# Performance work log

Measured on AMD Instinct MI355X. Metric: run time of the kernel, lower is better.

Reference implementation:

```python
import jax, jax.numpy as jnp
import numpy as np

N, D, H, E = 8192, 1024, 4096, 8
LN_EPS = 1e-5


def setup_inputs() -> dict:
    key = jax.random.key(0)
    ks = jax.random.split(key, 7)
    s_in = 1.0 / np.sqrt(D)
    s_hid = 1.0 / np.sqrt(H)
    return {
        "x": jax.random.normal(ks[0], (N, D), dtype=jnp.float32),
        "gate_w": jax.random.uniform(ks[1], (E, D), jnp.float32, -s_in, s_in),
        "gate_b": jax.random.uniform(ks[2], (E,), jnp.float32, -s_in, s_in),
        "w1": jax.random.uniform(ks[3], (E, H, D), jnp.float32, -s_in, s_in),
        "b1": jax.random.uniform(ks[4], (E, H), jnp.float32, -s_in, s_in),
        "w2": jax.random.uniform(ks[5], (E, D, H), jnp.float32, -s_hid, s_hid),
        "b2": jax.random.uniform(ks[6], (E, D), jnp.float32, -s_hid, s_hid),
        "ln_w": jnp.ones((D,), jnp.float32),
        "ln_b": jnp.zeros((D,), jnp.float32),
        "top_k": 2,
    }


def reference(x, gate_w, gate_b, w1, b1, w2, b2, ln_w, ln_b, top_k):
    # Gating: softmax over experts, then top-k, then renormalizing softmax over the k scores
    gate_scores = jax.nn.softmax(x @ gate_w.T + gate_b, axis=-1)          # [N, E]
    topk_scores, topk_idx = jax.lax.top_k(gate_scores, top_k)             # [N, K]
    topk_scores = jax.nn.softmax(topk_scores, axis=-1)                    # [N, K]

    # Dense all-expert FFN (matches original: every expert runs on every token)
    h = jax.nn.relu(jnp.einsum('nd,ehd->neh', x, w1) + b1)                # [N, E, H]
    y = jnp.einsum('neh,edh->ned', h, w2) + b2                            # [N, E, D]

    # Per-token gather of the top-k expert outputs and weighted combine
    sel = jnp.take_along_axis(y, topk_idx[:, :, None], axis=1)            # [N, K, D]
    moe_out = jnp.sum(topk_scores[:, :, None] * sel, axis=1)              # [N, D]

    # Residual + LayerNorm
    r = x + moe_out
    mu = jnp.mean(r, axis=-1, keepdims=True)
    var = jnp.mean(jnp.square(r - mu), axis=-1, keepdims=True)
    return (r - mu) * jax.lax.rsqrt(var + LN_EPS) * ln_w + ln_b
```

## Files before the change

kernel.cpp:

```cpp
#include <hip/hip_runtime.h>
#include <hip/hip_bf16.h>
#include <stdint.h>

#define N_TOK 8192
#define DIM 1024
#define HID 4096
#define NEXP 8
#define NSLOT 16384
#define NBLK 64

typedef __attribute__((ext_vector_type(8))) __bf16 bf16x8;
typedef __attribute__((ext_vector_type(4))) float f32x4;

__device__ __forceinline__ unsigned short f2bf(float f) {
  unsigned int u = __float_as_uint(f);
  u += 0x7fff + ((u >> 16) & 1);
  return (unsigned short)(u >> 16);
}
__device__ __forceinline__ float bf2f(unsigned short s) {
  return __uint_as_float(((unsigned int)s) << 16);
}
__device__ __forceinline__ void async16(const void* g, void* l) {
  __builtin_amdgcn_global_load_lds((__attribute__((address_space(1))) void*)(g),
                                   (__attribute__((address_space(3))) void*)(l), 16, 0, 0);
}
#define MFMA16(a, b, c) __builtin_amdgcn_mfma_f32_16x16x32_bf16(a, b, c, 0, 0, 0)

__global__ void cvt_kernel(const float* __restrict__ src, unsigned short* __restrict__ dst,
                           int n4) {
  int i = blockIdx.x * 256 + threadIdx.x;
  int stride = gridDim.x * 256;
  for (; i < n4; i += stride) {
    float4 v = ((const float4*)src)[i];
    ushort4 o;
    o.x = f2bf(v.x); o.y = f2bf(v.y); o.z = f2bf(v.z); o.w = f2bf(v.w);
    ((ushort4*)dst)[i] = o;
  }
}

__global__ void gate_kernel(const float* __restrict__ x, const float* __restrict__ gw,
                            const float* __restrict__ gb, int* __restrict__ expert2,
                            float* __restrict__ score2) {
  int token = blockIdx.x * 4 + (threadIdx.x >> 6);
  int lane = threadIdx.x & 63;
  const float4* xr = (const float4*)(x + (size_t)token * DIM);
  float acc[NEXP];
#pragma unroll
  for (int e = 0; e < NEXP; ++e) acc[e] = 0.f;
#pragma unroll
  for (int it = 0; it < DIM / 4 / 64; ++it) {
    int d = it * 64 + lane;
    float4 xv = xr[d];
#pragma unroll
    for (int e = 0; e < NEXP; ++e) {
      float4 wv = ((const float4*)(gw + e * DIM))[d];
      acc[e] += xv.x * wv.x + xv.y * wv.y + xv.z * wv.z + xv.w * wv.w;
    }
  }
#pragma unroll
  for (int off = 32; off > 0; off >>= 1) {
#pragma unroll
    for (int e = 0; e < NEXP; ++e) acc[e] += __shfl_xor(acc[e], off, 64);
  }
  if (lane == 0) {
    float lg[NEXP], mx = -1e30f;
#pragma unroll
    for (int e = 0; e < NEXP; ++e) { lg[e] = acc[e] + gb[e]; mx = fmaxf(mx, lg[e]); }
    float p[NEXP], s = 0.f;
#pragma unroll
    for (int e = 0; e < NEXP; ++e) { p[e] = expf(lg[e] - mx); s += p[e]; }
    float inv = 1.f / s;
#pragma unroll
    for (int e = 0; e < NEXP; ++e) p[e] *= inv;
    int i0 = 0;
#pragma unroll
    for (int e = 1; e < NEXP; ++e) if (p[e] > p[i0]) i0 = e;
    int i1 = (i0 == 0) ? 1 : 0;
#pragma unroll
    for (int e = 0; e < NEXP; ++e) if (e != i0 && p[e] > p[i1]) i1 = e;
    float eb = expf(p[i1] - p[i0]);
    float dn = 1.f / (1.f + eb);
    expert2[token * 2] = i0;
    expert2[token * 2 + 1] = i1;
    score2[token * 2] = dn;
    score2[token * 2 + 1] = eb * dn;
  }
}

__global__ void hist_kernel(const int* __restrict__ expert2, int* __restrict__ hist) {
  __shared__ int lh[NEXP];
  int b = blockIdx.x, t = threadIdx.x;
  if (t < NEXP) lh[t] = 0;
  __syncthreads();
  atomicAdd(&lh[expert2[b * 256 + t]], 1);
  __syncthreads();
  if (t < NEXP) hist[b * NEXP + t] = lh[t];
}

__global__ void scan_kernel(const int* __restrict__ hist, int* __restrict__ cnt,
                            int* __restrict__ off_, int* __restrict__ base) {
  __shared__ int lh[NBLK * NEXP];
  __shared__ int ltot[NEXP];
  __shared__ int loff[NEXP];
  int t = threadIdx.x;
#pragma unroll
  for (int e = 0; e < NEXP; ++e) lh[t * NEXP + e] = hist[t * NEXP + e];
  __syncthreads();
  if (t < NEXP) {
    int s = 0;
    for (int b = 0; b < NBLK; ++b) { int v = lh[b * NEXP + t]; lh[b * NEXP + t] = s; s += v; }
    ltot[t] = s;
  }
  __syncthreads();
  if (t == 0) {
    int s = 0;
#pragma unroll
    for (int e = 0; e < NEXP; ++e) { loff[e] = s; s += ltot[e]; }
  }
  __syncthreads();
  if (t < NEXP) { cnt[t] = ltot[t]; off_[t] = loff[t]; }
#pragma unroll
  for (int e = 0; e < NEXP; ++e) base[t * NEXP + e] = loff[e] + lh[t * NEXP + e];
}

__global__ void assign_kernel(const int* __restrict__ expert2, const int* __restrict__ base,
                              int* __restrict__ slot_of, int* __restrict__ token_of) {
  __shared__ int lh[NEXP];
  int b = blockIdx.x, t = threadIdx.x;
  if (t < NEXP) lh[t] = 0;
  __syncthreads();
  int i = b * 256 + t;
  int e = expert2[i];
  int r = atomicAdd(&lh[e], 1);
  int slot = base[b * NEXP + e] + r;
  slot_of[i] = slot;
  token_of[slot] = i >> 1;
}

__global__ void gather_kernel(const float* __restrict__ x, const int* __restrict__ token_of,
                              unsigned short* __restrict__ xg) {
  int slot = blockIdx.x;
  int t = threadIdx.x;
  int n = token_of[slot];
  float4 v = *(const float4*)(x + (size_t)n * DIM + t * 4);
  ushort4 o;
  o.x = f2bf(v.x); o.y = f2bf(v.y); o.z = f2bf(v.z); o.w = f2bf(v.w);
  *(ushort4*)(xg + (size_t)slot * DIM + t * 4) = o;
}

template <int KLEN, int NLEN, bool RELU>
__global__ __launch_bounds__(512, 2) void gemm_r3(
    const unsigned short* __restrict__ A, const unsigned short* __restrict__ B,
    const float* __restrict__ bias, unsigned short* __restrict__ C,
    const int* __restrict__ cnt, const int* __restrict__ off_) {
  const int NB_N = NLEN / 128;
  const int NT = KLEN / 64;
  int panel = blockIdx.z * 8 + blockIdx.x;
  int e = panel / NB_N;
  int n0 = (panel % NB_N) * 128;
  int me = cnt[e];
  int m0 = blockIdx.y * 256;
  if (m0 >= me) return;
  int rb = off_[e] + m0;

  __shared__ unsigned short lds_[73728];

  int tid = threadIdx.x;
  int wave = tid >> 6, lane = tid & 63;
  int wm = wave >> 1, wn = wave & 1;
  int quad = lane >> 4, l16 = lane & 15;
  int x7 = l16 & 7;

  int crow = tid >> 3, kc = tid & 7;
  int sslot = kc ^ (crow & 7);
  const char* Ab = (const char*)A;
  const char* Bb = (const char*)(B + (size_t)e * NLEN * KLEN);
  uint32_t aof[4], bof[2];
#pragma unroll
  for (int j = 0; j < 4; ++j) {
    int gr = rb + j * 64 + crow;
    gr = gr > NSLOT - 1 ? NSLOT - 1 : gr;
    aof[j] = (uint32_t)gr * (KLEN * 2) + sslot * 16;
  }
#pragma unroll
  for (int j = 0; j < 2; ++j)
    bof[j] = (uint32_t)(n0 + j * 64 + crow) * (KLEN * 2) + sslot * 16;

#define STG_A2(sbuf, kb, j0)                                                  \
  {                                                                           \
    async16(Ab + aof[j0] + (kb), &lds_[(sbuf) * 16384 + ((j0)*512 + tid) * 8]); \
    async16(Ab + aof[(j0) + 1] + (kb),                                        \
            &lds_[(sbuf) * 16384 + (((j0) + 1) * 512 + tid) * 8]);            \
  }
#define STG_B1(sbuf, kb, j)                                                   \
  async16(Bb + bof[j] + (kb), &lds_[49152 + (sbuf) * 8192 + ((j)*512 + tid) * 8]);

  f32x4 acc[4][4];
#pragma unroll
  for (int i = 0; i < 4; ++i)
#pragma unroll
    for (int j = 0; j < 4; ++j) acc[i][j] = {0.f, 0.f, 0.f, 0.f};

  STG_A2(0, 0, 0); STG_A2(0, 0, 2); STG_B1(0, 0, 0); STG_B1(0, 0, 1);
  STG_A2(1, 128, 0); STG_A2(1, 128, 2); STG_B1(1, 128, 0); STG_B1(1, 128, 1);
  asm volatile("s_waitcnt vmcnt(6)" ::: "memory");
  __builtin_amdgcn_sched_barrier(0);
  __builtin_amdgcn_s_barrier();

  const int abase = (wm * 64 + l16) * 64;
  const int bbase = (wn * 64 + l16) * 64;
  const int q0s = (quad ^ x7) * 8;
  const int q1s = ((4 + quad) ^ x7) * 8;

  int cur = 0;
#pragma unroll 1
  for (int t = 0; t < NT; ++t) {
    const int stg = (cur >= 1) ? cur - 1 : 2;
    const unsigned short* pa = &lds_[cur * 16384];
    const unsigned short* pb = &lds_[49152 + cur * 8192];
    const uint32_t kb2 = (uint32_t)(t + 2) << 7;
    const bool pre = (t + 2 < NT);
    bf16x8 a0[4], b0[4], a1[4], b1[4];
#pragma unroll
    for (int mt = 0; mt < 4; ++mt) a0[mt] = *(const bf16x8*)&pa[abase + mt * 1024 + q0s];
#pragma unroll
    for (int nt = 0; nt < 4; ++nt) b0[nt] = *(const bf16x8*)&pb[bbase + nt * 1024 + q0s];
    if (pre) { STG_A2(stg, kb2, 0); STG_B1(stg, kb2, 0); }
#pragma unroll
    for (int mt = 0; mt < 4; ++mt) a1[mt] = *(const bf16x8*)&pa[abase + mt * 1024 + q1s];
#pragma unroll
    for (int nt = 0; nt < 4; ++nt) b1[nt] = *(const bf16x8*)&pb[bbase + nt * 1024 + q1s];
    if (pre) { STG_A2(stg, kb2, 2); STG_B1(stg, kb2, 1); }
    asm volatile("s_waitcnt lgkmcnt(8)" ::: "memory");
    __builtin_amdgcn_sched_barrier(0);
    __builtin_amdgcn_s_setprio(1);
#pragma unroll
    for (int mt = 0; mt < 4; ++mt)
#pragma unroll
      for (int nt = 0; nt < 4; ++nt) acc[mt][nt] = MFMA16(a0[mt], b0[nt], acc[mt][nt]);
    __builtin_amdgcn_s_setprio(0);
    asm volatile("s_waitcnt lgkmcnt(0)" ::: "memory");
    __builtin_amdgcn_sched_barrier(0);
    __builtin_amdgcn_s_setprio(1);
#pragma unroll
    for (int mt = 0; mt < 4; ++mt)
#pragma unroll
      for (int nt = 0; nt < 4; ++nt) acc[mt][nt] = MFMA16(a1[mt], b1[nt], acc[mt][nt]);
    __builtin_amdgcn_s_setprio(0);
    if (t + 1 < NT) {
      if (pre) {
        asm volatile("s_waitcnt vmcnt(6)" ::: "memory");
      } else {
        asm volatile("s_waitcnt vmcnt(0)" ::: "memory");
      }
    }
    __builtin_amdgcn_sched_barrier(0);
    __builtin_amdgcn_s_barrier();
    cur = (cur == 2) ? 0 : cur + 1;
  }
#undef STG_A2
#undef STG_B1

#pragma unroll
  for (int mt = 0; mt < 4; ++mt) {
#pragma unroll
    for (int r = 0; r < 4; ++r) {
      int mrow = wm * 64 + mt * 16 + quad * 4 + r;
      if (m0 + mrow < me) {
#pragma unroll
        for (int nt = 0; nt < 4; ++nt) {
          int col = n0 + wn * 64 + nt * 16 + l16;
          float v = acc[mt][nt][r] + bias[e * NLEN + col];
          if (RELU) v = fmaxf(v, 0.f);
          C[(size_t)(rb + mrow) * NLEN + col] = f2bf(v);
        }
      }
    }
  }
}

template <int KLEN, int NLEN, bool RELU>
__global__ __launch_bounds__(256, 4) void gemm_bt(
    const unsigned short* __restrict__ A, const void* __restrict__ Bptr,
    const float* __restrict__ bias, unsigned short* __restrict__ C,
    const int* __restrict__ cnt, const int* __restrict__ off_) {
  const int NB_N = NLEN / 128;
  int panel = blockIdx.z * 8 + blockIdx.x;
  int e = panel / NB_N;
  int n0 = (panel % NB_N) * 128;
  int me = cnt[e];
  int m0 = blockIdx.y * 128;
  if (m0 >= me) return;
  int rb = off_[e] + m0;

  __shared__ unsigned short lA[8192];
  __shared__ unsigned short lB[8192];

  int tid = threadIdx.x;
  int wave = tid >> 6, lane = tid & 63;
  int wm = (wave >> 1) * 64, wn = (wave & 1) * 64;
  int quad = lane >> 4, l16 = lane & 15;
  int x7 = l16 & 7;

  int arow[4], brow[4], akx[4], ldst[4];
#pragma unroll
  for (int i = 0; i < 4; ++i) {
    int c = i * 256 + tid;
    int row = c >> 3;
    akx[i] = (c & 7) ^ (row & 7);
    ldst[i] = c * 8;
    brow[i] = row;
    int grow = rb + row;
    arow[i] = (grow > NSLOT - 1) ? (NSLOT - 1) : grow;
  }

  f32x4 acc[4][4];
#pragma unroll
  for (int i = 0; i < 4; ++i)
#pragma unroll
    for (int j = 0; j < 4; ++j) acc[i][j] = {0.f, 0.f, 0.f, 0.f};

  const float* Bf = (const float*)Bptr + (size_t)e * NLEN * KLEN;

  for (int k0 = 0; k0 < KLEN; k0 += 64) {
#pragma unroll
    for (int i = 0; i < 4; ++i)
      async16(A + (size_t)arow[i] * KLEN + k0 + akx[i] * 8, &lA[ldst[i]]);
#pragma unroll
    for (int i = 0; i < 4; ++i) {
      const float* gp = Bf + (size_t)(n0 + brow[i]) * KLEN + k0 + akx[i] * 8;
      float4 v0 = *(const float4*)gp;
      float4 v1 = *(const float4*)(gp + 4);
      union { unsigned short u[8]; bf16x8 v; } pk;
      pk.u[0] = f2bf(v0.x); pk.u[1] = f2bf(v0.y); pk.u[2] = f2bf(v0.z); pk.u[3] = f2bf(v0.w);
      pk.u[4] = f2bf(v1.x); pk.u[5] = f2bf(v1.y); pk.u[6] = f2bf(v1.z); pk.u[7] = f2bf(v1.w);
      *(bf16x8*)(&lB[ldst[i]]) = pk.v;
    }
    __syncthreads();
#pragma unroll
    for (int s = 0; s < 2; ++s) {
      int qx = (s * 4 + quad) ^ x7;
      bf16x8 af[4], bfr[4];
#pragma unroll
      for (int mt = 0; mt < 4; ++mt)
        af[mt] = *(const bf16x8*)(&lA[(wm + mt * 16 + l16) * 64 + qx * 8]);
#pragma unroll
      for (int nt = 0; nt < 4; ++nt)
        bfr[nt] = *(const bf16x8*)(&lB[(wn + nt * 16 + l16) * 64 + qx * 8]);
#pragma unroll
      for (int mt = 0; mt < 4; ++mt)
#pragma unroll
        for (int nt = 0; nt < 4; ++nt)
          acc[mt][nt] = MFMA16(af[mt], bfr[nt], acc[mt][nt]);
    }
    __syncthreads();
  }
#pragma unroll
  for (int mt = 0; mt < 4; ++mt) {
#pragma unroll
    for (int r = 0; r < 4; ++r) {
      int mrow = wm + mt * 16 + quad * 4 + r;
      if (m0 + mrow < me) {
#pragma unroll
        for (int nt = 0; nt < 4; ++nt) {
          int col = n0 + wn + nt * 16 + l16;
          float v = acc[mt][nt][r] + bias[e * NLEN + col];
          if (RELU) v = fmaxf(v, 0.f);
          C[(size_t)(rb + mrow) * NLEN + col] = f2bf(v);
        }
      }
    }
  }
}

__global__ void ln_kernel(const float* __restrict__ x, const unsigned short* __restrict__ y,
                          const int* __restrict__ slot_of, const float* __restrict__ score2,
                          const float* __restrict__ lnw, const float* __restrict__ lnb,
                          float* __restrict__ out) {
  __shared__ float red[8];
  int n = blockIdx.x, t = threadIdx.x;
  int wave = t >> 6, lane = t & 63;
  int s0 = slot_of[n * 2], s1 = slot_of[n * 2 + 1];
  float w0 = score2[n * 2], w1 = score2[n * 2 + 1];
  float4 xv = *(const float4*)(x + (size_t)n * DIM + t * 4);
  ushort4 y0 = *(const ushort4*)(y + (size_t)s0 * DIM + t * 4);
  ushort4 y1 = *(const ushort4*)(y + (size_t)s1 * DIM + t * 4);
  float r0 = xv.x + w0 * bf2f(y0.x) + w1 * bf2f(y1.x);
  float r1 = xv.y + w0 * bf2f(y0.y) + w1 * bf2f(y1.y);
  float r2 = xv.z + w0 * bf2f(y0.z) + w1 * bf2f(y1.z);
  float r3 = xv.w + w0 * bf2f(y0.w) + w1 * bf2f(y1.w);
  float sum = r0 + r1 + r2 + r3;
  float sq = r0 * r0 + r1 * r1 + r2 * r2 + r3 * r3;
#pragma unroll
  for (int off = 32; off > 0; off >>= 1) {
    sum += __shfl_xor(sum, off, 64);
    sq += __shfl_xor(sq, off, 64);
  }
  if (lane == 0) { red[wave] = sum; red[4 + wave] = sq; }
  __syncthreads();
  sum = red[0] + red[1] + red[2] + red[3];
  sq = red[4] + red[5] + red[6] + red[7];
  float mu = sum * (1.f / DIM);
  float var = sq * (1.f / DIM) - mu * mu;
  float rs = rsqrtf(var + 1e-5f);
  float4 wv = *(const float4*)(lnw + t * 4);
  float4 bv = *(const float4*)(lnb + t * 4);
  float4 o;
  o.x = (r0 - mu) * rs * wv.x + bv.x;
  o.y = (r1 - mu) * rs * wv.y + bv.y;
  o.z = (r2 - mu) * rs * wv.z + bv.z;
  o.w = (r3 - mu) * rs * wv.w + bv.w;
  *(float4*)(out + (size_t)n * DIM + t * 4) = o;
}

extern "C" void kernel_launch(void* const* d_in, const int* in_sizes, int n_in,
                              void* d_out, int out_size, void* d_ws, size_t ws_size,
                              hipStream_t stream) {
  const float* x = (const float*)d_in[0];
  const float* gw = (const float*)d_in[1];
  const float* gb = (const float*)d_in[2];
  const float* w1 = (const float*)d_in[3];
  const float* b1 = (const float*)d_in[4];
  const float* w2 = (const float*)d_in[5];
  const float* b2 = (const float*)d_in[6];
  const float* lnw = (const float*)d_in[7];
  const float* lnb = (const float*)d_in[8];
  float* out = (float*)d_out;
  char* ws = (char*)d_ws;

  int* cnt = (int*)(ws + 0);
  int* off_ = (int*)(ws + 64);
  int* hist = (int*)(ws + 4096);
  int* base = (int*)(ws + 4096 + 2048);
  int* expert2 = (int*)(ws + 65536);
  float* score2 = (float*)(ws + 2 * 65536);
  int* slot_of = (int*)(ws + 3 * 65536);
  int* token_of = (int*)(ws + 4 * 65536);
  const size_t XG_OFF = 524288;
  const size_t H_OFF = XG_OFF + (size_t)NSLOT * DIM * 2;
  const size_t Y_OFF = H_OFF + (size_t)NSLOT * HID * 2;
  const size_t WB1_OFF = Y_OFF + (size_t)NSLOT * DIM * 2;
  const size_t WB2_OFF = WB1_OFF + (size_t)NEXP * HID * DIM * 2;
  const size_t WS_NEED = WB2_OFF + (size_t)NEXP * DIM * HID * 2;
  unsigned short* xg = (unsigned short*)(ws + XG_OFF);
  unsigned short* h = (unsigned short*)(ws + H_OFF);
  unsigned short* y = (unsigned short*)(ws + Y_OFF);
  unsigned short* wb1 = (unsigned short*)(ws + WB1_OFF);
  unsigned short* wb2 = (unsigned short*)(ws + WB2_OFF);
  bool cvt_ok = ws_size >= WS_NEED;

  gate_kernel<<<N_TOK / 4, 256, 0, stream>>>(x, gw, gb, expert2, score2);
  hist_kernel<<<NBLK, 256, 0, stream>>>(expert2, hist);
  scan_kernel<<<1, 64, 0, stream>>>(hist, cnt, off_, base);
  assign_kernel<<<NBLK, 256, 0, stream>>>(expert2, base, slot_of, token_of);
  gather_kernel<<<NSLOT, 256, 0, stream>>>(x, token_of, xg);
  if (cvt_ok) {
    const int n4 = NEXP * HID * DIM / 4;
    cvt_kernel<<<4096, 256, 0, stream>>>(w1, wb1, n4);
    cvt_kernel<<<4096, 256, 0, stream>>>(w2, wb2, n4);
    gemm_r3<DIM, HID, true>
        <<<dim3(8, 64, (NEXP * HID / 128) / 8), 512, 0, stream>>>(xg, wb1, b1, h, cnt, off_);
    gemm_r3<HID, DIM, false>
        <<<dim3(8, 64, (NEXP * DIM / 128) / 8), 512, 0, stream>>>(h, wb2, b2, y, cnt, off_);
  } else {
    gemm_bt<DIM, HID, true>
        <<<dim3(8, 128, (NEXP * HID / 128) / 8), 256, 0, stream>>>(xg, w1, b1, h, cnt, off_);
    gemm_bt<HID, DIM, false>
        <<<dim3(8, 128, (NEXP * DIM / 128) / 8), 256, 0, stream>>>(h, w2, b2, y, cnt, off_);
  }
  ln_kernel<<<N_TOK, 256, 0, stream>>>(x, y, slot_of, score2, lnw, lnb, out);
}
```

Measured before the change: 786.5 us.

## Use four waves with 128x64 per-wave tiles in the expert GEMM

Rewrites the routed expert GEMM to launch 256 threads (four waves) instead of 512 for the same 256x128 block tile. Each wave now computes a 128x64 sub-tile with 8x4 MFMA accumulators, raising register-level reuse of the A and B fragments. All global-to-LDS async copies are issued after both LDS fragment reads, and the waitcnt thresholds are adjusted. The cost is higher register pressure, launch bounds that allow one block per CU, and fewer waves available to hide latency.

```diff
diff --git a/kernel.cpp b/kernel.cpp
--- a/kernel.cpp
+++ b/kernel.cpp
@@ -149,7 +149,7 @@
 }
 
 template <int KLEN, int NLEN, bool RELU>
-__global__ __launch_bounds__(512, 2) void gemm_r3(
+__global__ __launch_bounds__(256, 1) void gemm_w4(
     const unsigned short* __restrict__ A, const unsigned short* __restrict__ B,
     const float* __restrict__ bias, unsigned short* __restrict__ C,
     const int* __restrict__ cnt, const int* __restrict__ off_) {
@@ -175,39 +175,42 @@
   int sslot = kc ^ (crow & 7);
   const char* Ab = (const char*)A;
   const char* Bb = (const char*)(B + (size_t)e * NLEN * KLEN);
-  uint32_t aof[4], bof[2];
-#pragma unroll
-  for (int j = 0; j < 4; ++j) {
-    int gr = rb + j * 64 + crow;
+  uint32_t aof[8], bof[4];
+#pragma unroll
+  for (int j = 0; j < 8; ++j) {
+    int gr = rb + j * 32 + crow;
     gr = gr > NSLOT - 1 ? NSLOT - 1 : gr;
     aof[j] = (uint32_t)gr * (KLEN * 2) + sslot * 16;
   }
 #pragma unroll
-  for (int j = 0; j < 2; ++j)
-    bof[j] = (uint32_t)(n0 + j * 64 + crow) * (KLEN * 2) + sslot * 16;
-
-#define STG_A2(sbuf, kb, j0)                                                  \
-  {                                                                           \
-    async16(Ab + aof[j0] + (kb), &lds_[(sbuf) * 16384 + ((j0)*512 + tid) * 8]); \
-    async16(Ab + aof[(j0) + 1] + (kb),                                        \
-            &lds_[(sbuf) * 16384 + (((j0) + 1) * 512 + tid) * 8]);            \
-  }
-#define STG_B1(sbuf, kb, j)                                                   \
-  async16(Bb + bof[j] + (kb), &lds_[49152 + (sbuf) * 8192 + ((j)*512 + tid) * 8]);
-
-  f32x4 acc[4][4];
-#pragma unroll
-  for (int i = 0; i < 4; ++i)
+  for (int j = 0; j < 4; ++j)
+    bof[j] = (uint32_t)(n0 + j * 32 + crow) * (KLEN * 2) + sslot * 16;
+
+#define STG_A(sbuf, kb)                                                        \
+  {                                                                            \
+    _Pragma("unroll") for (int j = 0; j < 8; ++j)                              \
+        async16(Ab + aof[j] + (kb), &lds_[(sbuf) * 16384 + (j * 256 + tid) * 8]); \
+  }
+#define STG_B(sbuf, kb)                                                        \
+  {                                                                            \
+    _Pragma("unroll") for (int j = 0; j < 4; ++j)                              \
+        async16(Bb + bof[j] + (kb),                                            \
+                &lds_[49152 + (sbuf) * 8192 + (j * 256 + tid) * 8]);           \
+  }
+
+  f32x4 acc[8][4];
+#pragma unroll
+  for (int i = 0; i < 8; ++i)
 #pragma unroll
     for (int j = 0; j < 4; ++j) acc[i][j] = {0.f, 0.f, 0.f, 0.f};
 
-  STG_A2(0, 0, 0); STG_A2(0, 0, 2); STG_B1(0, 0, 0); STG_B1(0, 0, 1);
-  STG_A2(1, 128, 0); STG_A2(1, 128, 2); STG_B1(1, 128, 0); STG_B1(1, 128, 1);
-  asm volatile("s_waitcnt vmcnt(6)" ::: "memory");
+  STG_A(0, 0); STG_B(0, 0);
+  STG_A(1, 128); STG_B(1, 128);
+  asm volatile("s_waitcnt vmcnt(12)" ::: "memory");
   __builtin_amdgcn_sched_barrier(0);
   __builtin_amdgcn_s_barrier();
 
-  const int abase = (wm * 64 + l16) * 64;
+  const int abase = (wm * 128 + l16) * 64;
   const int bbase = (wn * 64 + l16) * 64;
   const int q0s = (quad ^ x7) * 8;
   const int q1s = ((4 + quad) ^ x7) * 8;
@@ -220,22 +223,23 @@
     const unsigned short* pb = &lds_[49152 + cur * 8192];
     const uint32_t kb2 = (uint32_t)(t + 2) << 7;
     const bool pre = (t + 2 < NT);
-    bf16x8 a0[4], b0[4], a1[4], b1[4];
-#pragma unroll
-    for (int mt = 0; mt < 4; ++mt) a0[mt] = *(const bf16x8*)&pa[abase + mt * 1024 + q0s];
+    bf16x8 a0[8], b0[4], a1[8], b1[4];
+#pragma unroll
+    for (int mt = 0; mt < 8; ++mt) a0[mt] = *(const bf16x8*)&pa[abase + mt * 1024 + q0s];
 #pragma unroll
     for (int nt = 0; nt < 4; ++nt) b0[nt] = *(const bf16x8*)&pb[bbase + nt * 1024 + q0s];
-    if (pre) { STG_A2(stg, kb2, 0); STG_B1(stg, kb2, 0); }
-#pragma unroll
-    for (int mt = 0; mt < 4; ++mt) a1[mt] = *(const bf16x8*)&pa[abase + mt * 1024 + q1s];
+    __builtin_amdgcn_sched_barrier(0);
+#pragma unroll
+    for (int mt = 0; mt < 8; ++mt) a1[mt] = *(const bf16x8*)&pa[abase + mt * 1024 + q1s];
 #pragma unroll
     for (int nt = 0; nt < 4; ++nt) b1[nt] = *(const bf16x8*)&pb[bbase + nt * 1024 + q1s];
-    if (pre) { STG_A2(stg, kb2, 2); STG_B1(stg, kb2, 1); }
-    asm volatile("s_waitcnt lgkmcnt(8)" ::: "memory");
+    if (pre) { STG_A(stg, kb2); STG_B(stg, kb2); }
+    __builtin_amdgcn_sched_barrier(0);
+    asm volatile("s_waitcnt lgkmcnt(12)" ::: "memory");
     __builtin_amdgcn_sched_barrier(0);
     __builtin_amdgcn_s_setprio(1);
 #pragma unroll
-    for (int mt = 0; mt < 4; ++mt)
+    for (int mt = 0; mt < 8; ++mt)
 #pragma unroll
       for (int nt = 0; nt < 4; ++nt) acc[mt][nt] = MFMA16(a0[mt], b0[nt], acc[mt][nt]);
     __builtin_amdgcn_s_setprio(0);
@@ -243,13 +247,13 @@
     __builtin_amdgcn_sched_barrier(0);
     __builtin_amdgcn_s_setprio(1);
 #pragma unroll
-    for (int mt = 0; mt < 4; ++mt)
+    for (int mt = 0; mt < 8; ++mt)
 #pragma unroll
       for (int nt = 0; nt < 4; ++nt) acc[mt][nt] = MFMA16(a1[mt], b1[nt], acc[mt][nt]);
     __builtin_amdgcn_s_setprio(0);
     if (t + 1 < NT) {
       if (pre) {
-        asm volatile("s_waitcnt vmcnt(6)" ::: "memory");
+        asm volatile("s_waitcnt vmcnt(12)" ::: "memory");
       } else {
         asm volatile("s_waitcnt vmcnt(0)" ::: "memory");
       }
@@ -258,14 +262,14 @@
     __builtin_amdgcn_s_barrier();
     cur = (cur == 2) ? 0 : cur + 1;
   }
-#undef STG_A2
-#undef STG_B1
-
-#pragma unroll
-  for (int mt = 0; mt < 4; ++mt) {
+#undef STG_A
+#undef STG_B
+
+#pragma unroll
+  for (int mt = 0; mt < 8; ++mt) {
 #pragma unroll
     for (int r = 0; r < 4; ++r) {
-      int mrow = wm * 64 + mt * 16 + quad * 4 + r;
+      int mrow = wm * 128 + mt * 16 + quad * 4 + r;
       if (m0 + mrow < me) {
 #pragma unroll
         for (int nt = 0; nt < 4; ++nt) {
@@ -458,10 +462,10 @@
     const int n4 = NEXP * HID * DIM / 4;
     cvt_kernel<<<4096, 256, 0, stream>>>(w1, wb1, n4);
     cvt_kernel<<<4096, 256, 0, stream>>>(w2, wb2, n4);
-    gemm_r3<DIM, HID, true>
-        <<<dim3(8, 64, (NEXP * HID / 128) / 8), 512, 0, stream>>>(xg, wb1, b1, h, cnt, off_);
-    gemm_r3<HID, DIM, false>
-        <<<dim3(8, 64, (NEXP * DIM / 128) / 8), 512, 0, stream>>>(h, wb2, b2, y, cnt, off_);
+    gemm_w4<DIM, HID, true>
+        <<<dim3(8, 64, (NEXP * HID / 128) / 8), 256, 0, stream>>>(xg, wb1, b1, h, cnt, off_);
+    gemm_w4<HID, DIM, false>
+        <<<dim3(8, 64, (NEXP * DIM / 128) / 8), 256, 0, stream>>>(h, wb2, b2, y, cnt, off_);
   } else {
     gemm_bt<DIM, HID, true>
         <<<dim3(8, 128, (NEXP * HID / 128) / 8), 256, 0, stream>>>(xg, w1, b1, h, cnt, off_);
```

Result: slower. 853.9 us (+8.6%).
